# Optimization experiments

Hardware: AMD Instinct MI355X
Metric: run time of the kernel (lower is better)

## Reference

```python
import jax, jax.numpy as jnp
import numpy as np
from jax import lax

N_STATES = 512
VOCAB = 32000
BATCH = 16
SEQ_LEN = 128


def setup_inputs() -> dict:
    key = jax.random.key(0)
    k_ids, k_em, k_tm, k_p = jax.random.split(key, 4)
    input_ids = jax.random.randint(k_ids, (BATCH, SEQ_LEN), 0, VOCAB, dtype=jnp.int64)
    em = jax.random.normal(k_em, (N_STATES, VOCAB), dtype=jnp.float32)
    tm = jax.random.normal(k_tm, (N_STATES, N_STATES), dtype=jnp.float32)
    p = jax.random.normal(k_p, (N_STATES,), dtype=jnp.float32)
    return {"input_ids": input_ids, "em": em, "tm": tm, "p": p}


def reference(input_ids, em, tm, p):
    """HMM forward algorithm in log space; returns mean NLL (scalar).

    em: [S, V] emission logits, tm: [S, S] transition logits, p: [S] prior logits.
    do_log_softmax=True -> normalize each in log space first.
    """
    log_em = jax.nn.log_softmax(em, axis=-1)   # [S, V]
    log_tm = jax.nn.log_softmax(tm, axis=-1)   # [S, S] rows = source state
    log_p = jax.nn.log_softmax(p, axis=-1)     # [S]

    # Gather emission log-probs per token: [B, T, S]
    em_tok = log_em.T[input_ids]

    # alpha_0[b, s] = log_p[s] + log_em[s, x_0]
    alpha0 = log_p[None, :] + em_tok[:, 0]     # [B, S]

    def step(alpha, e_t):
        # alpha: [B, S_src]; log-matmul: logsumexp over source states
        a = jax.nn.logsumexp(alpha[:, :, None] + log_tm[None, :, :], axis=1) + e_t
        return a, None

    em_rest = jnp.swapaxes(em_tok[:, 1:], 0, 1)  # [T-1, B, S]
    alpha_T, _ = lax.scan(step, alpha0, em_rest)

    # loss = -mean_b log p(x_b) = -mean_b logsumexp_s alpha_T[b, s]
    loss = -jnp.mean(jax.nn.logsumexp(alpha_T, axis=-1))
    return loss
```

## Files before the change

kernel.cpp:

```cpp
#include <hip/hip_runtime.h>
#include <hip/hip_bf16.h>

#define NS 512
#define NV 32000
#define NB 16
#define NT 128

#ifndef __has_builtin
#define __has_builtin(x) 0
#endif

typedef int v8i __attribute__((ext_vector_type(8)));
typedef float v4f __attribute__((ext_vector_type(4)));

__device__ inline unsigned enc_e4m3(float x) {
    x = fminf(x, 448.0f);
    unsigned u = __float_as_uint(x);
    if (x < 0.015625f) {
        return (unsigned)(int)rintf(x * 512.0f);
    }
    unsigned u2 = u + 0x7FFFFu + ((u >> 20) & 1u);
    return (((u2 >> 23) - 120u) << 3) | ((u2 >> 20) & 7u);
}

__device__ inline unsigned pack4_e4m3(float a, float b, float c, float d) {
#if __has_builtin(__builtin_amdgcn_cvt_pk_fp8_f32)
    int v = __builtin_amdgcn_cvt_pk_fp8_f32(a, b, 0, false);
    v = __builtin_amdgcn_cvt_pk_fp8_f32(c, d, v, true);
    return (unsigned)v;
#else
    return enc_e4m3(a) | (enc_e4m3(b) << 8) | (enc_e4m3(c) << 16) | (enc_e4m3(d) << 24);
#endif
}

#define DPPMAX(x, ctrl) \
    x = fmaxf(x, __int_as_float(__builtin_amdgcn_mov_dpp(__float_as_int(x), ctrl, 0xF, 0xF, true)))
#define DPPADD(x, ctrl) \
    x = x + __int_as_float(__builtin_amdgcn_mov_dpp(__float_as_int(x), ctrl, 0xF, 0xF, true))

__global__ __launch_bounds__(256) void k_emtok_T(
    const float* __restrict__ em, const int* __restrict__ ids,
    float* __restrict__ em_lin_T)
{
    const int s   = blockIdx.x;
    const int tid = threadIdx.x;
    const float* row = em + (size_t)s * NV;

    int idv[8];
#pragma unroll
    for (int k = 0; k < 8; ++k) idv[k] = ids[tid + 256 * k];
    float g[8];
#pragma unroll
    for (int k = 0; k < 8; ++k) g[k] = row[idv[k]];

    float sum = 0.f;
    const float4* row4 = (const float4*)row;
#pragma unroll 4
    for (int i = 0; i < 31; ++i) {
        float4 v = row4[tid + 256 * i];
        sum += __expf(v.x) + __expf(v.y) + __expf(v.z) + __expf(v.w);
    }
    sum += __expf(row[31744 + tid]);

#pragma unroll
    for (int off = 32; off; off >>= 1) sum += __shfl_down(sum, off);
    __shared__ float red[4];
    __shared__ float s_scale;
    if ((tid & 63) == 0) red[tid >> 6] = sum;
    __syncthreads();
    if (tid == 0) s_scale = (1.0f / ((red[0] + red[1]) + (red[2] + red[3]))) * 0x1p-18f;
    __syncthreads();
    const float scale = s_scale;

#pragma unroll
    for (int k = 0; k < 8; ++k)
        em_lin_T[(size_t)s * (NB * NT) + tid + 256 * k] = __expf(g[k]) * scale;
}

__global__ __launch_bounds__(256) void k_tr(
    const float* __restrict__ emT, float* __restrict__ em_lin)
{
    __shared__ float tile[32][33];
    const int jb = blockIdx.x * 32;
    const int sb = blockIdx.y * 32;
    const int cc = threadIdx.x & 31;
    const int rr = threadIdx.x >> 5;
#pragma unroll
    for (int i = 0; i < 4; ++i) {
        int r = rr + 8 * i;
        tile[r][cc] = emT[(size_t)(sb + r) * (NB * NT) + jb + cc];
    }
    __syncthreads();
#pragma unroll
    for (int i = 0; i < 4; ++i) {
        int r = rr + 8 * i;
        em_lin[(size_t)(jb + r) * NS + sb + cc] = tile[cc][r];
    }
}

__global__ __launch_bounds__(64) void k_z(
    const float* __restrict__ tm, float* __restrict__ zscale)
{
    const int k    = blockIdx.x;
    const int lane = threadIdx.x;
    const float* row = tm + (size_t)k * NS;

    float4 a = ((const float4*)row)[lane * 2];
    float4 b = ((const float4*)row)[lane * 2 + 1];
    float sum = ((__expf(a.x) + __expf(a.y)) + (__expf(a.z) + __expf(a.w)))
              + ((__expf(b.x) + __expf(b.y)) + (__expf(b.z) + __expf(b.w)));
#pragma unroll
    for (int off = 32; off; off >>= 1) sum += __shfl_down(sum, off);
    if (lane == 0) zscale[k] = 1024.0f / sum;
}

__global__ __launch_bounds__(256) void k_pt2(
    const float* __restrict__ tm, const float* __restrict__ zscale,
    unsigned char* __restrict__ PT)
{
    __shared__ float tile[64][65];
    __shared__ float zs[64];
    const int kb  = blockIdx.x * 64;
    const int db  = blockIdx.y * 64;
    const int tid = threadIdx.x;
    const int c   = tid & 63;
    const int r0  = tid >> 6;

    if (tid < 64) zs[tid] = zscale[kb + tid];
#pragma unroll
    for (int i = 0; i < 16; ++i) {
        int r = r0 + 4 * i;
        tile[r][c] = tm[(size_t)(kb + r) * NS + db + c];
    }
    __syncthreads();

    const int d  = tid >> 2;
    const int ks = (tid & 3) * 16;
    unsigned px[4];
#pragma unroll
    for (int gq = 0; gq < 4; ++gq) {
        int k0 = ks + gq * 4;
        px[gq] = pack4_e4m3(__expf(tile[k0 + 0][d]) * zs[k0 + 0],
                            __expf(tile[k0 + 1][d]) * zs[k0 + 1],
                            __expf(tile[k0 + 2][d]) * zs[k0 + 2],
                            __expf(tile[k0 + 3][d]) * zs[k0 + 3]);
    }
    uint4 o; o.x = px[0]; o.y = px[1]; o.z = px[2]; o.w = px[3];
    *(uint4*)(PT + (size_t)(db + d) * NS + kb + ks) = o;
}

__global__ __launch_bounds__(512, 2) void k_scan(
    const float* __restrict__ em_lin, const unsigned char* __restrict__ PT,
    const float* __restrict__ p, float* __restrict__ out)
{
    const int bb  = blockIdx.x;
    const int tid = threadIdx.x;
    const int w   = tid >> 6;
    const int l   = tid & 63;
    const int lc  = l & 15;
    const int lq  = l >> 4;

    __shared__ unsigned Ew[16 * 128];
    __shared__ unsigned wmE[8][4];
    __shared__ unsigned mbuf[4];
    __shared__ float    wm2[8][4];
    __shared__ float    sbuf[4];

    v8i B[4][4];
#pragma unroll
    for (int nt = 0; nt < 4; ++nt) {
#pragma unroll
        for (int kt = 0; kt < 4; ++kt) {
            const uint4* src = (const uint4*)(PT + (size_t)((w * 4 + nt) * 16 + lc) * NS + kt * 128 + lq * 32);
            uint4 lo = src[0], hi = src[1];
            v8i bb8;
            bb8[0] = (int)lo.x; bb8[1] = (int)lo.y; bb8[2] = (int)lo.z; bb8[3] = (int)lo.w;
            bb8[4] = (int)hi.x; bb8[5] = (int)hi.y; bb8[6] = (int)hi.z; bb8[7] = (int)hi.w;
            B[nt][kt] = bb8;
        }
    }

    float zp = 0.f;
#pragma unroll
    for (int i = 0; i < 8; ++i) zp += __expf(p[l * 8 + i]);
    DPPADD(zp, 0x128); DPPADD(zp, 0x124); DPPADD(zp, 0xB1); DPPADD(zp, 0x4E);
    float Zp = __int_as_float(__builtin_amdgcn_readlane(__float_as_int(zp), 0))
             + __int_as_float(__builtin_amdgcn_readlane(__float_as_int(zp), 16))
             + __int_as_float(__builtin_amdgcn_readlane(__float_as_int(zp), 32))
             + __int_as_float(__builtin_amdgcn_readlane(__float_as_int(zp), 48));
    const float invZp = 1.0f / Zp;

    const int dbase0 = w * 64 + lc;
    const int gb     = bb * 4 + lq;

    const float* epb0 = em_lin + (size_t)gb * (NT * NS) + dbase0;
    float alpha[4];
#pragma unroll
    for (int nt = 0; nt < 4; ++nt)
        alpha[nt] = __expf(p[dbase0 + 16 * nt]) * invZp * epb0[16 * nt];

    int gsum = 18;
    const unsigned sel1 = (l & 1) ? 0x07030501u : 0x02060004u;
    const unsigned sel2 = (l & 2) ? 0x07060302u : 0x01000504u;
    const int mrow = 4 * lq + (l & 3);

    int aidx[8];
#pragma unroll
    for (int kt = 0; kt < 4; ++kt) {
#pragma unroll
        for (int c = 0; c < 2; ++c)
            aidx[kt * 2 + c] = lc * 32 + (((kt * 8 + lq * 2 + c) ^ lc) & 31);
    }
    int widx[4];
#pragma unroll
    for (int nt = 0; nt < 4; ++nt)
        widx[nt] = mrow * 128 + ((((w * 4 + nt) ^ mrow) & 31) << 2) + (lc >> 2);

    const float* epb = epb0 + NS;

    for (int t = 1; t < NT; ++t) {
        float epf[4];
#pragma unroll
        for (int nt = 0; nt < 4; ++nt) epf[nt] = epb[16 * nt];
        epb += NS;

        float mx = fmaxf(fmaxf(alpha[0], alpha[1]), fmaxf(alpha[2], alpha[3]));
        DPPMAX(mx, 0x128); DPPMAX(mx, 0x124); DPPMAX(mx, 0xB1); DPPMAX(mx, 0x4E);
        if (lc == 0) wmE[w][lq] = __float_as_uint(mx) >> 23;
        __syncthreads();

        if (tid < 4) {
            unsigned e0 = wmE[0][tid], e1 = wmE[1][tid], e2 = wmE[2][tid], e3 = wmE[3][tid];
            unsigned e4 = wmE[4][tid], e5 = wmE[5][tid], e6 = wmE[6][tid], e7 = wmE[7][tid];
            unsigned m01 = e0 > e1 ? e0 : e1,  m23 = e2 > e3 ? e2 : e3;
            unsigned m45 = e4 > e5 ? e4 : e5,  m67 = e6 > e7 ? e6 : e7;
            unsigned ma = m01 > m23 ? m01 : m23, mb = m45 > m67 ? m45 : m67;
            mbuf[tid] = ma > mb ? ma : mb;
        }
        __syncthreads();

        const unsigned eb = mbuf[lq];
        const float sc = __uint_as_float((261u - eb) << 23);
        gsum += (int)eb - 126;

#pragma unroll
        for (int nt = 0; nt < 4; ++nt) {
            unsigned dw = pack4_e4m3(alpha[nt] * sc, 0.f, 0.f, 0.f);
            int tmp = __builtin_amdgcn_mov_dpp((int)dw, 0xB1, 0xF, 0xF, true);
            dw = __builtin_amdgcn_perm(dw, (unsigned)tmp, sel1);
            tmp = __builtin_amdgcn_mov_dpp((int)dw, 0x4E, 0xF, 0xF, true);
            dw = __builtin_amdgcn_perm(dw, (unsigned)tmp, sel2);
            Ew[widx[nt]] = dw;
        }
        __syncthreads();

        v8i A[4];
        const uint4* eb4 = (const uint4*)&Ew[0];
#pragma unroll
        for (int kt = 0; kt < 4; ++kt) {
            uint4 lo = eb4[aidx[kt * 2 + 0]];
            uint4 hi = eb4[aidx[kt * 2 + 1]];
            v8i aa;
            aa[0] = (int)lo.x; aa[1] = (int)lo.y; aa[2] = (int)lo.z; aa[3] = (int)lo.w;
            aa[4] = (int)hi.x; aa[5] = (int)hi.y; aa[6] = (int)hi.z; aa[7] = (int)hi.w;
            A[kt] = aa;
        }

        v4f C[4];
#pragma unroll
        for (int nt = 0; nt < 4; ++nt) { C[nt][0] = 0.f; C[nt][1] = 0.f; C[nt][2] = 0.f; C[nt][3] = 0.f; }
#pragma unroll
        for (int kt = 0; kt < 4; ++kt)
#pragma unroll
            for (int nt = 0; nt < 4; ++nt)
                C[nt] = __builtin_amdgcn_mfma_scale_f32_16x16x128_f8f6f4(
                            A[kt], B[nt][kt], C[nt], 0, 0, 0, 0x7F7F7F7F, 0, 0x7F7F7F7F);

#pragma unroll
        for (int nt = 0; nt < 4; ++nt)
            alpha[nt] = C[nt][0] * epf[nt];
    }

    {
        float sm = (alpha[0] + alpha[1]) + (alpha[2] + alpha[3]);
        DPPADD(sm, 0x128); DPPADD(sm, 0x124); DPPADD(sm, 0xB1); DPPADD(sm, 0x4E);
        if (lc == 0) wm2[w][lq] = sm;
        if (w == 0 && lc == 0) sbuf[lq] = (float)gsum;
    }
    __syncthreads();
    if (tid < 4) {
        float s8 = ((wm2[0][tid] + wm2[1][tid]) + (wm2[2][tid] + wm2[3][tid]))
                 + ((wm2[4][tid] + wm2[5][tid]) + (wm2[6][tid] + wm2[7][tid]));
        float L2 = __log2f(s8) + sbuf[tid];
        atomicAdd(out, -(0.693147180559945f / 16.0f) * L2);
    }
}

extern "C" void kernel_launch(void* const* d_in, const int* in_sizes, int n_in,
                              void* d_out, int out_size, void* d_ws, size_t ws_size,
                              hipStream_t stream)
{
    const int*   ids = (const int*)d_in[0];
    const float* em  = (const float*)d_in[1];
    const float* tm  = (const float*)d_in[2];
    const float* p   = (const float*)d_in[3];
    float* out = (float*)d_out;

    float*          em_lin = (float*)d_ws;
    unsigned char*  PT     = (unsigned char*)d_ws + ((size_t)4 << 20);
    float*          zscale = (float*)((unsigned char*)d_ws + ((size_t)4 << 20) + ((size_t)256 << 10));
    float*          emT    = (float*)((unsigned char*)d_ws + ((size_t)4 << 20) + ((size_t)512 << 10));

    hipMemsetAsync(d_out, 0, sizeof(float), stream);

    k_emtok_T<<<NS, 256, 0, stream>>>(em, ids, emT);
    k_tr<<<dim3(64, 16), 256, 0, stream>>>(emT, em_lin);
    k_z<<<NS, 64, 0, stream>>>(tm, zscale);
    k_pt2<<<dim3(8, 8), 256, 0, stream>>>(tm, zscale, PT);
    k_scan<<<4, 512, 0, stream>>>(em_lin, PT, p, out);
}
```

Before: 244.7 us.

## Merge setup kernels into two launches and restructure scan A-tile layout

Replaces the four preprocessing kernels with two. The first computes the emission row sums and the transition normalizers. The second gathers token emissions directly with exp and transpose, and also builds the FP8 transition matrix. This removes launches and the intermediate emT buffer. The scan kernel is restructured so only 16 lanes per wave hold four batch rows each. It computes per-row maxima with one barrier plus a direct read instead of the tid<4 reduction stage, and uses a padded LDS layout for the A operand. The cost is more per-lane work on fewer lanes and serialized setup dependencies.

```diff
diff --git a/kernel.cpp b/kernel.cpp
--- a/kernel.cpp
+++ b/kernel.cpp
@@ -38,118 +38,101 @@
 #define DPPADD(x, ctrl) \
     x = x + __int_as_float(__builtin_amdgcn_mov_dpp(__float_as_int(x), ctrl, 0xF, 0xF, true))
 
-__global__ __launch_bounds__(256) void k_emtok_T(
-    const float* __restrict__ em, const int* __restrict__ ids,
-    float* __restrict__ em_lin_T)
+__global__ __launch_bounds__(256) void k_setup1(
+    const float* __restrict__ em, const float* __restrict__ tm,
+    float* __restrict__ scaleZ, float* __restrict__ zscale)
 {
-    const int s   = blockIdx.x;
+    const int b   = blockIdx.x;
     const int tid = threadIdx.x;
-    const float* row = em + (size_t)s * NV;
-
-    int idv[8];
-#pragma unroll
-    for (int k = 0; k < 8; ++k) idv[k] = ids[tid + 256 * k];
-    float g[8];
-#pragma unroll
-    for (int k = 0; k < 8; ++k) g[k] = row[idv[k]];
-
-    float sum = 0.f;
-    const float4* row4 = (const float4*)row;
+    __shared__ float red[4];
+
+    if (b < NS) {
+        const float* row = em + (size_t)b * NV;
+        float sum = 0.f;
+        const float4* row4 = (const float4*)row;
 #pragma unroll 4
-    for (int i = 0; i < 31; ++i) {
-        float4 v = row4[tid + 256 * i];
-        sum += __expf(v.x) + __expf(v.y) + __expf(v.z) + __expf(v.w);
-    }
-    sum += __expf(row[31744 + tid]);
-
-#pragma unroll
-    for (int off = 32; off; off >>= 1) sum += __shfl_down(sum, off);
-    __shared__ float red[4];
-    __shared__ float s_scale;
-    if ((tid & 63) == 0) red[tid >> 6] = sum;
-    __syncthreads();
-    if (tid == 0) s_scale = (1.0f / ((red[0] + red[1]) + (red[2] + red[3]))) * 0x1p-18f;
-    __syncthreads();
-    const float scale = s_scale;
-
-#pragma unroll
-    for (int k = 0; k < 8; ++k)
-        em_lin_T[(size_t)s * (NB * NT) + tid + 256 * k] = __expf(g[k]) * scale;
-}
-
-__global__ __launch_bounds__(256) void k_tr(
-    const float* __restrict__ emT, float* __restrict__ em_lin)
-{
-    __shared__ float tile[32][33];
-    const int jb = blockIdx.x * 32;
-    const int sb = blockIdx.y * 32;
-    const int cc = threadIdx.x & 31;
-    const int rr = threadIdx.x >> 5;
-#pragma unroll
-    for (int i = 0; i < 4; ++i) {
-        int r = rr + 8 * i;
-        tile[r][cc] = emT[(size_t)(sb + r) * (NB * NT) + jb + cc];
-    }
-    __syncthreads();
-#pragma unroll
-    for (int i = 0; i < 4; ++i) {
-        int r = rr + 8 * i;
-        em_lin[(size_t)(jb + r) * NS + sb + cc] = tile[cc][r];
-    }
-}
-
-__global__ __launch_bounds__(64) void k_z(
-    const float* __restrict__ tm, float* __restrict__ zscale)
-{
-    const int k    = blockIdx.x;
-    const int lane = threadIdx.x;
-    const float* row = tm + (size_t)k * NS;
-
-    float4 a = ((const float4*)row)[lane * 2];
-    float4 b = ((const float4*)row)[lane * 2 + 1];
-    float sum = ((__expf(a.x) + __expf(a.y)) + (__expf(a.z) + __expf(a.w)))
-              + ((__expf(b.x) + __expf(b.y)) + (__expf(b.z) + __expf(b.w)));
-#pragma unroll
-    for (int off = 32; off; off >>= 1) sum += __shfl_down(sum, off);
-    if (lane == 0) zscale[k] = 1024.0f / sum;
-}
-
-__global__ __launch_bounds__(256) void k_pt2(
-    const float* __restrict__ tm, const float* __restrict__ zscale,
+        for (int i = 0; i < 31; ++i) {
+            float4 v = row4[tid + 256 * i];
+            sum += __expf(v.x) + __expf(v.y) + __expf(v.z) + __expf(v.w);
+        }
+        sum += __expf(row[31744 + tid]);
+#pragma unroll
+        for (int off = 32; off; off >>= 1) sum += __shfl_down(sum, off);
+        if ((tid & 63) == 0) red[tid >> 6] = sum;
+        __syncthreads();
+        if (tid == 0) scaleZ[b] = 0x1p-18f / ((red[0] + red[1]) + (red[2] + red[3]));
+    } else {
+        const int k = b - NS;
+        const float* row = tm + (size_t)k * NS;
+        float2 v = ((const float2*)row)[tid];
+        float sum = __expf(v.x) + __expf(v.y);
+#pragma unroll
+        for (int off = 32; off; off >>= 1) sum += __shfl_down(sum, off);
+        if ((tid & 63) == 0) red[tid >> 6] = sum;
+        __syncthreads();
+        if (tid == 0) zscale[k] = 1024.0f / ((red[0] + red[1]) + (red[2] + red[3]));
+    }
+}
+
+__global__ __launch_bounds__(256) void k_setup2(
+    const float* __restrict__ em, const float* __restrict__ tm,
+    const int* __restrict__ ids, const float* __restrict__ scaleZ,
+    const float* __restrict__ zscale, float* __restrict__ em_lin,
     unsigned char* __restrict__ PT)
 {
-    __shared__ float tile[64][65];
+    const int b   = blockIdx.x;
+    const int tid = threadIdx.x;
+    __shared__ float tile[32][33];
+    __shared__ float tile2[64][65];
     __shared__ float zs[64];
-    const int kb  = blockIdx.x * 64;
-    const int db  = blockIdx.y * 64;
-    const int tid = threadIdx.x;
-    const int c   = tid & 63;
-    const int r0  = tid >> 6;
-
-    if (tid < 64) zs[tid] = zscale[kb + tid];
-#pragma unroll
-    for (int i = 0; i < 16; ++i) {
-        int r = r0 + 4 * i;
-        tile[r][c] = tm[(size_t)(kb + r) * NS + db + c];
-    }
-    __syncthreads();
-
-    const int d  = tid >> 2;
-    const int ks = (tid & 3) * 16;
-    unsigned px[4];
-#pragma unroll
-    for (int gq = 0; gq < 4; ++gq) {
-        int k0 = ks + gq * 4;
-        px[gq] = pack4_e4m3(__expf(tile[k0 + 0][d]) * zs[k0 + 0],
-                            __expf(tile[k0 + 1][d]) * zs[k0 + 1],
-                            __expf(tile[k0 + 2][d]) * zs[k0 + 2],
-                            __expf(tile[k0 + 3][d]) * zs[k0 + 3]);
-    }
-    uint4 o; o.x = px[0]; o.y = px[1]; o.z = px[2]; o.w = px[3];
-    *(uint4*)(PT + (size_t)(db + d) * NS + kb + ks) = o;
-}
-
-__global__ __launch_bounds__(512, 2) void k_scan(
+
+    if (b < 1024) {
+        const int jb = (b & 63) * 32;
+        const int sb = (b >> 6) * 32;
+        const int cc = tid & 31;
+        const int rr = tid >> 5;
+        const int tok = ids[jb + cc];
+#pragma unroll
+        for (int i = 0; i < 4; ++i) {
+            int s = sb + rr + 8 * i;
+            tile[rr + 8 * i][cc] = __expf(em[(size_t)s * NV + tok]) * scaleZ[s];
+        }
+        __syncthreads();
+#pragma unroll
+        for (int i = 0; i < 4; ++i) {
+            int r = rr + 8 * i;
+            em_lin[(size_t)(jb + r) * NS + sb + cc] = tile[cc][r];
+        }
+    } else {
+        const int pb = b - 1024;
+        const int kb = (pb & 7) * 64;
+        const int db = (pb >> 3) * 64;
+        const int c  = tid & 63;
+        const int r0 = tid >> 6;
+        if (tid < 64) zs[tid] = zscale[kb + tid];
+#pragma unroll
+        for (int i = 0; i < 16; ++i) {
+            int r = r0 + 4 * i;
+            tile2[r][c] = tm[(size_t)(kb + r) * NS + db + c];
+        }
+        __syncthreads();
+        const int d  = tid >> 2;
+        const int ks = (tid & 3) * 16;
+        unsigned px[4];
+#pragma unroll
+        for (int gq = 0; gq < 4; ++gq) {
+            int k0 = ks + gq * 4;
+            px[gq] = pack4_e4m3(__expf(tile2[k0 + 0][d]) * zs[k0 + 0],
+                                __expf(tile2[k0 + 1][d]) * zs[k0 + 1],
+                                __expf(tile2[k0 + 2][d]) * zs[k0 + 2],
+                                __expf(tile2[k0 + 3][d]) * zs[k0 + 3]);
+        }
+        uint4 o; o.x = px[0]; o.y = px[1]; o.z = px[2]; o.w = px[3];
+        *(uint4*)(PT + (size_t)(db + d) * NS + kb + ks) = o;
+    }
+}
+
+__global__ __launch_bounds__(512, 1) void k_scan(
     const float* __restrict__ em_lin, const unsigned char* __restrict__ PT,
     const float* __restrict__ p, float* __restrict__ out)
 {
@@ -160,11 +143,11 @@
     const int lc  = l & 15;
     const int lq  = l >> 4;
 
-    __shared__ unsigned Ew[16 * 128];
-    __shared__ unsigned wmE[8][4];
-    __shared__ unsigned mbuf[4];
-    __shared__ float    wm2[8][4];
-    __shared__ float    sbuf[4];
+    __shared__ __align__(16) unsigned EwD[16 * 132];
+    __shared__ float4 wm8[8];
+    __shared__ float4 sgf;
+
+    for (int i = tid; i < 16 * 132; i += 512) EwD[i] = 0u;
 
     v8i B[4][4];
 #pragma unroll
@@ -190,76 +173,90 @@
              + __int_as_float(__builtin_amdgcn_readlane(__float_as_int(zp), 48));
     const float invZp = 1.0f / Zp;
 
-    const int dbase0 = w * 64 + lc;
-    const int gb     = bb * 4 + lq;
-
-    const float* epb0 = em_lin + (size_t)gb * (NT * NS) + dbase0;
-    float alpha[4];
-#pragma unroll
-    for (int nt = 0; nt < 4; ++nt)
-        alpha[nt] = __expf(p[dbase0 + 16 * nt]) * invZp * epb0[16 * nt];
-
-    int gsum = 18;
+    const int d0 = w * 64 + lc;
+
+    float av[4][4];
+    const float* ep[4];
+    if (l < 16) {
+#pragma unroll
+        for (int r = 0; r < 4; ++r)
+            ep[r] = em_lin + (size_t)(bb * 4 + r) * (NT * NS) + d0;
+#pragma unroll
+        for (int nt = 0; nt < 4; ++nt) {
+            float pl = __expf(p[d0 + 16 * nt]) * invZp;
+#pragma unroll
+            for (int r = 0; r < 4; ++r)
+                av[nt][r] = pl * ep[r][16 * nt];
+        }
+#pragma unroll
+        for (int r = 0; r < 4; ++r) ep[r] += NS;
+    }
+    __syncthreads();
+
+    int gsum[4] = {18, 18, 18, 18};
     const unsigned sel1 = (l & 1) ? 0x07030501u : 0x02060004u;
     const unsigned sel2 = (l & 2) ? 0x07060302u : 0x01000504u;
-    const int mrow = 4 * lq + (l & 3);
-
-    int aidx[8];
-#pragma unroll
-    for (int kt = 0; kt < 4; ++kt) {
-#pragma unroll
-        for (int c = 0; c < 2; ++c)
-            aidx[kt * 2 + c] = lc * 32 + (((kt * 8 + lq * 2 + c) ^ lc) & 31);
-    }
-    int widx[4];
-#pragma unroll
-    for (int nt = 0; nt < 4; ++nt)
-        widx[nt] = mrow * 128 + ((((w * 4 + nt) ^ mrow) & 31) << 2) + (lc >> 2);
-
-    const float* epb = epb0 + NS;
+    const uint4* eb4 = (const uint4*)&EwD[0];
 
     for (int t = 1; t < NT; ++t) {
-        float epf[4];
-#pragma unroll
-        for (int nt = 0; nt < 4; ++nt) epf[nt] = epb[16 * nt];
-        epb += NS;
-
-        float mx = fmaxf(fmaxf(alpha[0], alpha[1]), fmaxf(alpha[2], alpha[3]));
-        DPPMAX(mx, 0x128); DPPMAX(mx, 0x124); DPPMAX(mx, 0xB1); DPPMAX(mx, 0x4E);
-        if (lc == 0) wmE[w][lq] = __float_as_uint(mx) >> 23;
-        __syncthreads();
-
-        if (tid < 4) {
-            unsigned e0 = wmE[0][tid], e1 = wmE[1][tid], e2 = wmE[2][tid], e3 = wmE[3][tid];
-            unsigned e4 = wmE[4][tid], e5 = wmE[5][tid], e6 = wmE[6][tid], e7 = wmE[7][tid];
-            unsigned m01 = e0 > e1 ? e0 : e1,  m23 = e2 > e3 ? e2 : e3;
-            unsigned m45 = e4 > e5 ? e4 : e5,  m67 = e6 > e7 ? e6 : e7;
-            unsigned ma = m01 > m23 ? m01 : m23, mb = m45 > m67 ? m45 : m67;
-            mbuf[tid] = ma > mb ? ma : mb;
-        }
-        __syncthreads();
-
-        const unsigned eb = mbuf[lq];
-        const float sc = __uint_as_float((261u - eb) << 23);
-        gsum += (int)eb - 126;
-
-#pragma unroll
-        for (int nt = 0; nt < 4; ++nt) {
-            unsigned dw = pack4_e4m3(alpha[nt] * sc, 0.f, 0.f, 0.f);
-            int tmp = __builtin_amdgcn_mov_dpp((int)dw, 0xB1, 0xF, 0xF, true);
-            dw = __builtin_amdgcn_perm(dw, (unsigned)tmp, sel1);
-            tmp = __builtin_amdgcn_mov_dpp((int)dw, 0x4E, 0xF, 0xF, true);
-            dw = __builtin_amdgcn_perm(dw, (unsigned)tmp, sel2);
-            Ew[widx[nt]] = dw;
+        float epf[4][4];
+        if (l < 16) {
+#pragma unroll
+            for (int nt = 0; nt < 4; ++nt)
+#pragma unroll
+                for (int r = 0; r < 4; ++r)
+                    epf[nt][r] = ep[r][16 * nt];
+#pragma unroll
+            for (int r = 0; r < 4; ++r) ep[r] += NS;
+        }
+
+        if (l < 16) {
+            float m0 = fmaxf(fmaxf(av[0][0], av[1][0]), fmaxf(av[2][0], av[3][0]));
+            float m1 = fmaxf(fmaxf(av[0][1], av[1][1]), fmaxf(av[2][1], av[3][1]));
+            float m2 = fmaxf(fmaxf(av[0][2], av[1][2]), fmaxf(av[2][2], av[3][2]));
+            float m3 = fmaxf(fmaxf(av[0][3], av[1][3]), fmaxf(av[2][3], av[3][3]));
+            DPPMAX(m0, 0x128); DPPMAX(m0, 0x124); DPPMAX(m0, 0xB1); DPPMAX(m0, 0x4E);
+            DPPMAX(m1, 0x128); DPPMAX(m1, 0x124); DPPMAX(m1, 0xB1); DPPMAX(m1, 0x4E);
+            DPPMAX(m2, 0x128); DPPMAX(m2, 0x124); DPPMAX(m2, 0xB1); DPPMAX(m2, 0x4E);
+            DPPMAX(m3, 0x128); DPPMAX(m3, 0x124); DPPMAX(m3, 0xB1); DPPMAX(m3, 0x4E);
+            if (l == 0) wm8[w] = make_float4(m0, m1, m2, m3);
+        }
+        __syncthreads();
+
+        if (l < 16) {
+            float4 m4 = wm8[0];
+#pragma unroll
+            for (int j = 1; j < 8; ++j) {
+                float4 v = wm8[j];
+                m4.x = fmaxf(m4.x, v.x); m4.y = fmaxf(m4.y, v.y);
+                m4.z = fmaxf(m4.z, v.z); m4.w = fmaxf(m4.w, v.w);
+            }
+            float mb[4] = {m4.x, m4.y, m4.z, m4.w};
+            float sc[4];
+#pragma unroll
+            for (int r = 0; r < 4; ++r) {
+                unsigned ebx = __float_as_uint(mb[r]) >> 23;
+                sc[r] = __uint_as_float((261u - ebx) << 23);
+                gsum[r] += (int)ebx - 126;
+            }
+#pragma unroll
+            for (int nt = 0; nt < 4; ++nt) {
+                unsigned dw = pack4_e4m3(av[nt][0] * sc[0], av[nt][1] * sc[1],
+                                         av[nt][2] * sc[2], av[nt][3] * sc[3]);
+                int tmp = __builtin_amdgcn_mov_dpp((int)dw, 0xB1, 0xF, 0xF, true);
+                dw = __builtin_amdgcn_perm(dw, (unsigned)tmp, sel1);
+                tmp = __builtin_amdgcn_mov_dpp((int)dw, 0x4E, 0xF, 0xF, true);
+                dw = __builtin_amdgcn_perm(dw, (unsigned)tmp, sel2);
+                EwD[(l & 3) * 132 + w * 16 + nt * 4 + (lc >> 2)] = dw;
+            }
         }
         __syncthreads();
 
         v8i A[4];
-        const uint4* eb4 = (const uint4*)&Ew[0];
 #pragma unroll
         for (int kt = 0; kt < 4; ++kt) {
-            uint4 lo = eb4[aidx[kt * 2 + 0]];
-            uint4 hi = eb4[aidx[kt * 2 + 1]];
+            uint4 lo = eb4[lc * 33 + kt * 8 + lq * 2];
+            uint4 hi = eb4[lc * 33 + kt * 8 + lq * 2 + 1];
             v8i aa;
             aa[0] = (int)lo.x; aa[1] = (int)lo.y; aa[2] = (int)lo.z; aa[3] = (int)lo.w;
             aa[4] = (int)hi.x; aa[5] = (int)hi.y; aa[6] = (int)hi.z; aa[7] = (int)hi.w;
@@ -276,22 +273,34 @@
                 C[nt] = __builtin_amdgcn_mfma_scale_f32_16x16x128_f8f6f4(
                             A[kt], B[nt][kt], C[nt], 0, 0, 0, 0x7F7F7F7F, 0, 0x7F7F7F7F);
 
-#pragma unroll
-        for (int nt = 0; nt < 4; ++nt)
-            alpha[nt] = C[nt][0] * epf[nt];
-    }
-
-    {
-        float sm = (alpha[0] + alpha[1]) + (alpha[2] + alpha[3]);
-        DPPADD(sm, 0x128); DPPADD(sm, 0x124); DPPADD(sm, 0xB1); DPPADD(sm, 0x4E);
-        if (lc == 0) wm2[w][lq] = sm;
-        if (w == 0 && lc == 0) sbuf[lq] = (float)gsum;
+        if (l < 16) {
+#pragma unroll
+            for (int nt = 0; nt < 4; ++nt)
+#pragma unroll
+                for (int r = 0; r < 4; ++r)
+                    av[nt][r] = C[nt][r] * epf[nt][r];
+        }
+    }
+
+    if (l < 16) {
+        float s0 = (av[0][0] + av[1][0]) + (av[2][0] + av[3][0]);
+        float s1 = (av[0][1] + av[1][1]) + (av[2][1] + av[3][1]);
+        float s2 = (av[0][2] + av[1][2]) + (av[2][2] + av[3][2]);
+        float s3 = (av[0][3] + av[1][3]) + (av[2][3] + av[3][3]);
+        DPPADD(s0, 0x128); DPPADD(s0, 0x124); DPPADD(s0, 0xB1); DPPADD(s0, 0x4E);
+        DPPADD(s1, 0x128); DPPADD(s1, 0x124); DPPADD(s1, 0xB1); DPPADD(s1, 0x4E);
+        DPPADD(s2, 0x128); DPPADD(s2, 0x124); DPPADD(s2, 0xB1); DPPADD(s2, 0x4E);
+        DPPADD(s3, 0x128); DPPADD(s3, 0x124); DPPADD(s3, 0xB1); DPPADD(s3, 0x4E);
+        if (l == 0) wm8[w] = make_float4(s0, s1, s2, s3);
+        if (tid == 0)
+            sgf = make_float4((float)gsum[0], (float)gsum[1], (float)gsum[2], (float)gsum[3]);
     }
     __syncthreads();
     if (tid < 4) {
-        float s8 = ((wm2[0][tid] + wm2[1][tid]) + (wm2[2][tid] + wm2[3][tid]))
-                 + ((wm2[4][tid] + wm2[5][tid]) + (wm2[6][tid] + wm2[7][tid]));
-        float L2 = __log2f(s8) + sbuf[tid];
+        float s8 = 0.f;
+#pragma unroll
+        for (int j = 0; j < 8; ++j) s8 += ((const float*)&wm8[j])[tid];
+        float L2 = __log2f(s8) + ((const float*)&sgf)[tid];
         atomicAdd(out, -(0.693147180559945f / 16.0f) * L2);
     }
 }
@@ -309,13 +318,11 @@
     float*          em_lin = (float*)d_ws;
     unsigned char*  PT     = (unsigned char*)d_ws + ((size_t)4 << 20);
     float*          zscale = (float*)((unsigned char*)d_ws + ((size_t)4 << 20) + ((size_t)256 << 10));
-    float*          emT    = (float*)((unsigned char*)d_ws + ((size_t)4 << 20) + ((size_t)512 << 10));
+    float*          scaleZ = (float*)((unsigned char*)d_ws + ((size_t)4 << 20) + ((size_t)260 << 10));
 
     hipMemsetAsync(d_out, 0, sizeof(float), stream);
 
-    k_emtok_T<<<NS, 256, 0, stream>>>(em, ids, emT);
-    k_tr<<<dim3(64, 16), 256, 0, stream>>>(emT, em_lin);
-    k_z<<<NS, 64, 0, stream>>>(tm, zscale);
-    k_pt2<<<dim3(8, 8), 256, 0, stream>>>(tm, zscale, PT);
+    k_setup1<<<1024, 256, 0, stream>>>(em, tm, scaleZ, zscale);
+    k_setup2<<<1088, 256, 0, stream>>>(em, tm, ids, scaleZ, zscale, em_lin, PT);
     k_scan<<<4, 512, 0, stream>>>(em_lin, PT, p, out);
 }
```

Measured after the change: 330.7 us. 1.35x slower.
